# Kernel tuning notes

Hardware: AMD Instinct MI355X
Metric: run time of the kernel (lower is better)

Reference implementation:

```python
import jax, jax.numpy as jnp
import numpy as np

B, C_IN, C_OUT, H, W = 32, 256, 256, 56, 56
RATE = 0.5
K = int(C_OUT * (1.0 - RATE))  # 128 channels zeroed
BN_EPS = 1e-5


def setup_inputs() -> dict:
    key = jax.random.key(0)
    ks = jax.random.split(key, 4)
    return {
        "x": jax.random.normal(ks[0], (B, C_IN, H, W), dtype=jnp.float32),
        "conv_w": jax.random.normal(ks[1], (C_OUT, C_IN, 3, 3), dtype=jnp.float32) * 0.05,
        "gate_w": jax.random.normal(ks[2], (C_OUT, C_IN), dtype=jnp.float32) * 0.05,
        "gate_b": jnp.ones((C_OUT,), dtype=jnp.float32),
        "bn_gamma": jnp.ones((C_OUT,), dtype=jnp.float32),
        "bn_beta": jnp.zeros((C_OUT,), dtype=jnp.float32),
        "bn_mean": jnp.zeros((C_OUT,), dtype=jnp.float32),
        "bn_var": jnp.ones((C_OUT,), dtype=jnp.float32),
    }


def reference(x, conv_w, gate_w, gate_b, bn_gamma, bn_beta, bn_mean, bn_var):
    # conv2: 3x3, stride 1, padding 1, no bias  -> [B, C_OUT, H, W]
    y = jax.lax.conv_general_dilated(
        x, conv_w, window_strides=(1, 1), padding=((1, 1), (1, 1)),
        dimension_numbers=("NCHW", "OIHW", "NCHW"))
    # BatchNorm2d (eval mode: running stats)
    inv = bn_gamma / jnp.sqrt(bn_var + BN_EPS)
    y = y * inv[None, :, None, None] + (bn_beta - bn_mean * inv)[None, :, None, None]
    # use_relu=True
    y = jax.nn.relu(y)
    # gate: global abs-avg-pool -> linear -> relu   [B, C_OUT]
    s = jnp.mean(jnp.abs(x), axis=(2, 3))  # [B, C_IN]
    g = jax.nn.relu(s @ gate_w.T + gate_b)
    # zero the K smallest gate values per row (topk of -g), then renormalize
    _, idx = jax.lax.top_k(-g, K)  # indices of K smallest
    t = g.at[jnp.arange(B)[:, None], idx].set(0.0)
    t = t / jnp.sum(t, axis=1, keepdims=True) * C_OUT
    # broadcast channel mask
    return y * t[:, :, None, None]
```

## Files before the change

kernel.cpp:

```cpp
#include <hip/hip_runtime.h>
#include <hip/hip_bf16.h>
#include <cstdint>

typedef unsigned short ushort_t;
typedef unsigned int uint_t;
typedef __bf16 bf16x8 __attribute__((ext_vector_type(8)));
typedef float f32x4 __attribute__((ext_vector_type(4)));

#define B_SZ 32
#define C_IN 256
#define C_OUT 256
#define H_SZ 56
#define W_SZ 56
#define HW 3136
#define HP 58
#define WP 58
#define BN_EPS 1e-5f
#define K_ZERO 128

__device__ __forceinline__ ushort_t f2bf(float f) {
    unsigned int u = __builtin_bit_cast(unsigned int, f);
    unsigned int r = (u + 0x7fffu + ((u >> 16) & 1u)) >> 16;
    return (ushort_t)r;
}

__device__ __forceinline__ void load_lds16(const void* gptr, void* ldsptr) {
    __builtin_amdgcn_global_load_lds(
        (const __attribute__((address_space(1))) unsigned int*)(uintptr_t)gptr,
        (__attribute__((address_space(3))) unsigned int*)(uintptr_t)ldsptr,
        16, 0, 0);
}

__global__ __launch_bounds__(256) void prep_w_kernel(const float* __restrict__ w,
                                                     const float* __restrict__ gamma,
                                                     const float* __restrict__ beta,
                                                     const float* __restrict__ mean,
                                                     const float* __restrict__ var,
                                                     ushort_t* __restrict__ Wt,
                                                     float* __restrict__ bninv,
                                                     float* __restrict__ bnadd,
                                                     float* __restrict__ s) {
    int idx = blockIdx.x * 256 + threadIdx.x;
    if (idx < 9 * C_OUT * C_IN) {
        int tap = idx >> 16;
        int rem = idx & 65535;
        int co = rem >> 8, ci = rem & 255;
        Wt[idx] = f2bf(w[(size_t)(co * C_IN + ci) * 9 + tap]);
    }
    if (blockIdx.x < 32) s[idx] = 0.f;
    if (blockIdx.x == 32 && threadIdx.x < C_OUT) {
        int c = threadIdx.x;
        float inv = gamma[c] * rsqrtf(var[c] + BN_EPS);
        bninv[c] = inv;
        bnadd[c] = beta[c] - mean[c] * inv;
    }
}

__global__ __launch_bounds__(256) void prep_x_kernel(const float* __restrict__ x,
                                                     ushort_t* __restrict__ xbp,
                                                     float* __restrict__ s) {
    const int cit = blockIdx.x, h = blockIdx.y, b = blockIdx.z;
    __shared__ float tile[64][57];
    __shared__ float red2[256];
    const int t = threadIdx.x;
    const float* src = x + ((size_t)(b * C_IN + cit * 64) * H_SZ + h) * W_SZ;
    for (int i = t; i < 64 * 14; i += 256) {
        int ci = i / 14, w4 = (i - ci * 14) * 4;
        float4 v = *(const float4*)(src + (size_t)ci * HW + w4);
        tile[ci][w4] = v.x; tile[ci][w4 + 1] = v.y;
        tile[ci][w4 + 2] = v.z; tile[ci][w4 + 3] = v.w;
    }
    __syncthreads();
    {
        int ci = t & 63, wg = t >> 6;
        float a = 0.f;
#pragma unroll
        for (int j = 0; j < 14; j++) a += fabsf(tile[ci][wg * 14 + j]);
        red2[t] = a;
    }
    __syncthreads();
    if (t < 64) {
        float tot = red2[t] + red2[t + 64] + red2[t + 128] + red2[t + 192];
        atomicAdd(&s[b * C_IN + cit * 64 + t], tot * (1.0f / (float)HW));
    }
    const uint2 z2 = make_uint2(0u, 0u);
    for (int i = t; i < W_SZ * 16; i += 256) {
        int w = i >> 4, c4 = (i & 15) * 4;
        uint_t lo = (uint_t)f2bf(tile[c4][w])     | ((uint_t)f2bf(tile[c4 + 1][w]) << 16);
        uint_t hi = (uint_t)f2bf(tile[c4 + 2][w]) | ((uint_t)f2bf(tile[c4 + 3][w]) << 16);
        size_t dst = ((size_t)((b * HP + h + 1) * WP + (w + 1))) * C_IN + cit * 64 + c4;
        *(uint2*)&xbp[dst] = make_uint2(lo, hi);
    }
    if (t < 32) {
        int side = t >> 4, c4 = (t & 15) * 4;
        size_t dst = ((size_t)((b * HP + h + 1) * WP + side * 57)) * C_IN + cit * 64 + c4;
        *(uint2*)&xbp[dst] = z2;
    }
    if (h == 0 || h == 55) {
        int prow = (h == 0) ? 0 : 57;
        for (int i = t; i < 58 * 16; i += 256) {
            int w = i >> 4, c4 = (i & 15) * 4;
            size_t dst = ((size_t)((b * HP + prow) * WP + w)) * C_IN + cit * 64 + c4;
            *(uint2*)&xbp[dst] = z2;
        }
    }
}

__global__ __launch_bounds__(256) void gate_kernel(const float* __restrict__ s,
                                                   const float* __restrict__ gw,
                                                   const float* __restrict__ gb,
                                                   float* __restrict__ tscale) {
    const int b = blockIdx.x, t = threadIdx.x;
    __shared__ float sh_s[C_IN], sh_g[C_OUT], red[256];
    sh_s[t] = s[b * C_IN + t];
    __syncthreads();
    float acc = gb[t];
    const float* wr = gw + (size_t)t * C_IN;
    for (int ci = 0; ci < C_IN; ci++) acc += sh_s[ci] * wr[ci];
    float g = fmaxf(acc, 0.f);
    sh_g[t] = g;
    __syncthreads();
    int cnt = 0;
    for (int j = 0; j < C_OUT; j++) {
        float gj = sh_g[j];
        cnt += (gj < g) || (gj == g && j < t);
    }
    float tv = (cnt >= K_ZERO) ? g : 0.f;
    red[t] = tv;
    __syncthreads();
    for (int off = 128; off > 0; off >>= 1) {
        if (t < off) red[t] += red[t + off];
        __syncthreads();
    }
    tscale[b * C_OUT + t] = tv * ((float)C_OUT / red[0]);
}

__global__ __launch_bounds__(256, 3) void conv_kernel(const ushort_t* __restrict__ xbp,
                                                      const ushort_t* __restrict__ Wt,
                                                      const float* __restrict__ bninv,
                                                      const float* __restrict__ bnadd,
                                                      const float* __restrict__ tscale,
                                                      float* __restrict__ out) {
    __shared__ __align__(16) ushort_t As[128 * 64];
    __shared__ __align__(16) ushort_t Bs[128 * 64];
    const int t = threadIdx.x;
    const int bxr = blockIdx.x;
    const int bx = (bxr >> 4) * 8 + (bxr & 7);
    const int by = (bxr >> 3) & 1;
    const int lane = t & 63;
    const int wv = t >> 6;
    const int waveM = wv >> 1, waveN = wv & 1;

    const int srow = t >> 3;
    const int gxor8 = ((t & 7) ^ (srow & 7)) * 8;
    int arow[4], wrow[4];
#pragma unroll
    for (int i = 0; i < 4; i++) {
        int p = bx * 128 + i * 32 + srow;
        int b = p / HW;
        int r = p - b * HW;
        int hh = r / W_SZ, ww = r - hh * W_SZ;
        arow[i] = ((b * HP + hh + 1) * WP + (ww + 1)) * C_IN + gxor8;
        wrow[i] = (by * 128 + i * 32 + srow) * C_IN + gxor8;
    }
    ushort_t* ldsA = As + t * 8;
    ushort_t* ldsB = Bs + t * 8;

    int aoff[2][4], boff[2][4];
#pragma unroll
    for (int ks = 0; ks < 2; ks++) {
        int c = (lane >> 4) + ks * 4;
#pragma unroll
        for (int mt = 0; mt < 4; mt++) {
            int ra = waveM * 64 + mt * 16 + (lane & 15);
            aoff[ks][mt] = (ra * 8 + (c ^ (ra & 7))) * 16;
            int rb = waveN * 64 + mt * 16 + (lane & 15);
            boff[ks][mt] = (rb * 8 + (c ^ (rb & 7))) * 16;
        }
    }

    f32x4 acc[4][4];
#pragma unroll
    for (int i = 0; i < 4; i++)
#pragma unroll
        for (int j = 0; j < 4; j++) acc[i][j] = (f32x4){0.f, 0.f, 0.f, 0.f};

    const char* Ab = (const char*)As;
    const char* Bb = (const char*)Bs;

    for (int tap = 0; tap < 9; tap++) {
        const int doff = ((tap / 3 - 1) * WP + (tap % 3 - 1)) * C_IN;
        const int woff = tap * (C_OUT * C_IN);
#pragma unroll
        for (int cq = 0; cq < 4; cq++) {
            const int ci0 = cq * 64;
#pragma unroll
            for (int i = 0; i < 4; i++) {
                load_lds16(xbp + arow[i] + doff + ci0, ldsA + i * 2048);
                load_lds16(Wt + wrow[i] + woff + ci0, ldsB + i * 2048);
            }
            __syncthreads();
#pragma unroll
            for (int ks = 0; ks < 2; ks++) {
                bf16x8 af[4], bf[4];
#pragma unroll
                for (int mt = 0; mt < 4; mt++) af[mt] = *(const bf16x8*)(Ab + aoff[ks][mt]);
#pragma unroll
                for (int nt = 0; nt < 4; nt++) bf[nt] = *(const bf16x8*)(Bb + boff[ks][nt]);
#pragma unroll
                for (int mt = 0; mt < 4; mt++)
#pragma unroll
                    for (int nt = 0; nt < 4; nt++)
                        acc[mt][nt] = __builtin_amdgcn_mfma_f32_16x16x32_bf16(
                            af[mt], bf[nt], acc[mt][nt], 0, 0, 0);
            }
            __syncthreads();
        }
    }

#pragma unroll
    for (int mt = 0; mt < 4; mt++) {
        int p0 = bx * 128 + waveM * 64 + mt * 16 + (lane >> 4) * 4;
        int b = p0 / HW;
        int hw = p0 - b * HW;
#pragma unroll
        for (int nt = 0; nt < 4; nt++) {
            int co = by * 128 + waveN * 64 + nt * 16 + (lane & 15);
            float inv = bninv[co], add = bnadd[co], tsc = tscale[b * C_OUT + co];
            float4 o;
            o.x = fmaxf(acc[mt][nt][0] * inv + add, 0.f) * tsc;
            o.y = fmaxf(acc[mt][nt][1] * inv + add, 0.f) * tsc;
            o.z = fmaxf(acc[mt][nt][2] * inv + add, 0.f) * tsc;
            o.w = fmaxf(acc[mt][nt][3] * inv + add, 0.f) * tsc;
            *(float4*)(out + (size_t)(b * C_OUT + co) * HW + hw) = o;
        }
    }
}

extern "C" void kernel_launch(void* const* d_in, const int* in_sizes, int n_in,
                              void* d_out, int out_size, void* d_ws, size_t ws_size,
                              hipStream_t stream) {
    const float* x      = (const float*)d_in[0];
    const float* conv_w = (const float*)d_in[1];
    const float* gate_w = (const float*)d_in[2];
    const float* gate_b = (const float*)d_in[3];
    const float* bn_g   = (const float*)d_in[4];
    const float* bn_b   = (const float*)d_in[5];
    const float* bn_m   = (const float*)d_in[6];
    const float* bn_v   = (const float*)d_in[7];
    float* out = (float*)d_out;

    char* ws = (char*)d_ws;
    float*    s      = (float*)(ws + 0);
    float*    tscale = (float*)(ws + 32768);
    float*    bninv  = (float*)(ws + 65536);
    float*    bnadd  = (float*)(ws + 66560);
    ushort_t* Wt     = (ushort_t*)(ws + 67584);
    ushort_t* xbp    = (ushort_t*)(ws + 1247232);

    prep_w_kernel<<<2304, 256, 0, stream>>>(conv_w, bn_g, bn_b, bn_m, bn_v, Wt, bninv, bnadd, s);
    prep_x_kernel<<<dim3(4, 56, 32), 256, 0, stream>>>(x, xbp, s);
    gate_kernel<<<32, 256, 0, stream>>>(s, gate_w, gate_b, tscale);
    conv_kernel<<<1568, 256, 0, stream>>>(xbp, Wt, bninv, bnadd, tscale, out);
}
```

Baseline: 350.4 us.

## Reuse a padded input window in LDS across all nine conv taps

Each block now loads a 256-row window of padded input pixels for a 64-channel slice once, then runs all nine taps from shared memory by shifting the row offset. Before, the A tile was reloaded from global for every tap. Tiles no longer cross image boundaries: each image is split into 25 tiles, giving 1600 blocks, with a guard on the output store. The cost is a larger LDS footprint, which may cut occupancy, an extra barrier per tap for weight reloads, and some wasted rows in the last tile of each image.

Result: slower. 363.7 us (+3.8%).

```diff
diff --git a/kernel.cpp b/kernel.cpp
--- a/kernel.cpp
+++ b/kernel.cpp
@@ -15,6 +15,7 @@
 #define HW 3136
 #define HP 58
 #define WP 58
+#define HPWP 3364
 #define BN_EPS 1e-5f
 #define K_ZERO 128
 
@@ -141,41 +142,51 @@
                                                       const float* __restrict__ bnadd,
                                                       const float* __restrict__ tscale,
                                                       float* __restrict__ out) {
-    __shared__ __align__(16) ushort_t As[128 * 64];
+    __shared__ __align__(16) ushort_t Aw[256 * 64];
     __shared__ __align__(16) ushort_t Bs[128 * 64];
     const int t = threadIdx.x;
     const int bxr = blockIdx.x;
     const int bx = (bxr >> 4) * 8 + (bxr & 7);
     const int by = (bxr >> 3) & 1;
+    const int b = bx / 25;
+    const int ti = bx - b * 25;
     const int lane = t & 63;
     const int wv = t >> 6;
     const int waveM = wv >> 1, waveN = wv & 1;
 
+    const int r0 = ti * 128;
+    const int h0 = r0 / W_SZ, w0 = r0 - h0 * W_SZ;
+    const int padp0 = (h0 + 1) * WP + (w0 + 1);
+    const int g0l = min(padp0 - 59, HPWP - 256);
+
     const int srow = t >> 3;
     const int gxor8 = ((t & 7) ^ (srow & 7)) * 8;
-    int arow[4], wrow[4];
-#pragma unroll
-    for (int i = 0; i < 4; i++) {
-        int p = bx * 128 + i * 32 + srow;
-        int b = p / HW;
-        int r = p - b * HW;
+    const size_t abase = ((size_t)b * HPWP + g0l + srow) * C_IN + gxor8;
+    int wrowB[4];
+#pragma unroll
+    for (int i = 0; i < 4; i++)
+        wrowB[i] = (by * 128 + i * 32 + srow) * C_IN + gxor8;
+    ushort_t* ldsA = Aw + t * 8;
+    ushort_t* ldsB = Bs + t * 8;
+
+    int o_mt[4];
+#pragma unroll
+    for (int mt = 0; mt < 4; mt++) {
+        int r = r0 + waveM * 64 + mt * 16 + (lane & 15);
+        if (r >= HW) r = HW - 1;
         int hh = r / W_SZ, ww = r - hh * W_SZ;
-        arow[i] = ((b * HP + hh + 1) * WP + (ww + 1)) * C_IN + gxor8;
-        wrow[i] = (by * 128 + i * 32 + srow) * C_IN + gxor8;
-    }
-    ushort_t* ldsA = As + t * 8;
-    ushort_t* ldsB = Bs + t * 8;
-
-    int aoff[2][4], boff[2][4];
+        o_mt[mt] = (hh + 1) * WP + (ww + 1) - g0l;
+    }
+    const int q4 = (lane >> 4);
+
+    int boff[2][4];
 #pragma unroll
     for (int ks = 0; ks < 2; ks++) {
-        int c = (lane >> 4) + ks * 4;
-#pragma unroll
-        for (int mt = 0; mt < 4; mt++) {
-            int ra = waveM * 64 + mt * 16 + (lane & 15);
-            aoff[ks][mt] = (ra * 8 + (c ^ (ra & 7))) * 16;
-            int rb = waveN * 64 + mt * 16 + (lane & 15);
-            boff[ks][mt] = (rb * 8 + (c ^ (rb & 7))) * 16;
+        int c = q4 + ks * 4;
+#pragma unroll
+        for (int nt = 0; nt < 4; nt++) {
+            int rb = waveN * 64 + nt * 16 + (lane & 15);
+            boff[ks][nt] = (rb * 8 + (c ^ (rb & 7))) * 16;
         }
     }
 
@@ -185,28 +196,36 @@
 #pragma unroll
         for (int j = 0; j < 4; j++) acc[i][j] = (f32x4){0.f, 0.f, 0.f, 0.f};
 
-    const char* Ab = (const char*)As;
+    const char* Ab = (const char*)Aw;
     const char* Bb = (const char*)Bs;
 
-    for (int tap = 0; tap < 9; tap++) {
-        const int doff = ((tap / 3 - 1) * WP + (tap % 3 - 1)) * C_IN;
-        const int woff = tap * (C_OUT * C_IN);
-#pragma unroll
-        for (int cq = 0; cq < 4; cq++) {
-            const int ci0 = cq * 64;
-#pragma unroll
-            for (int i = 0; i < 4; i++) {
-                load_lds16(xbp + arow[i] + doff + ci0, ldsA + i * 2048);
-                load_lds16(Wt + wrow[i] + woff + ci0, ldsB + i * 2048);
-            }
-            __syncthreads();
+    for (int cq = 0; cq < 4; cq++) {
+        const int ci0 = cq * 64;
+#pragma unroll
+        for (int i = 0; i < 8; i++)
+            load_lds16(xbp + abase + (size_t)i * (32 * C_IN) + ci0, ldsA + i * 2048);
+#pragma unroll
+        for (int i = 0; i < 4; i++)
+            load_lds16(Wt + wrowB[i] + ci0, ldsB + i * 2048);
+        __syncthreads();
+
+        for (int tap = 0; tap < 9; tap++) {
+            const int dlt = (tap / 3 - 1) * WP + (tap % 3 - 1);
+            int aoff0[4];
+#pragma unroll
+            for (int mt = 0; mt < 4; mt++) {
+                int sp = o_mt[mt] + dlt;
+                aoff0[mt] = sp * 128 + ((q4 ^ (sp & 7)) << 4);
+            }
 #pragma unroll
             for (int ks = 0; ks < 2; ks++) {
                 bf16x8 af[4], bf[4];
 #pragma unroll
-                for (int mt = 0; mt < 4; mt++) af[mt] = *(const bf16x8*)(Ab + aoff[ks][mt]);
-#pragma unroll
-                for (int nt = 0; nt < 4; nt++) bf[nt] = *(const bf16x8*)(Bb + boff[ks][nt]);
+                for (int mt = 0; mt < 4; mt++)
+                    af[mt] = *(const bf16x8*)(Ab + (aoff0[mt] ^ (ks << 6)));
+#pragma unroll
+                for (int nt = 0; nt < 4; nt++)
+                    bf[nt] = *(const bf16x8*)(Bb + boff[ks][nt]);
 #pragma unroll
                 for (int mt = 0; mt < 4; mt++)
 #pragma unroll
@@ -215,24 +234,31 @@
                             af[mt], bf[nt], acc[mt][nt], 0, 0, 0);
             }
             __syncthreads();
+            if (tap < 8) {
+                const int woff = (tap + 1) * (C_OUT * C_IN) + ci0;
+#pragma unroll
+                for (int i = 0; i < 4; i++)
+                    load_lds16(Wt + wrowB[i] + woff, ldsB + i * 2048);
+                __syncthreads();
+            }
         }
     }
 
 #pragma unroll
     for (int mt = 0; mt < 4; mt++) {
-        int p0 = bx * 128 + waveM * 64 + mt * 16 + (lane >> 4) * 4;
-        int b = p0 / HW;
-        int hw = p0 - b * HW;
-#pragma unroll
-        for (int nt = 0; nt < 4; nt++) {
-            int co = by * 128 + waveN * 64 + nt * 16 + (lane & 15);
-            float inv = bninv[co], add = bnadd[co], tsc = tscale[b * C_OUT + co];
-            float4 o;
-            o.x = fmaxf(acc[mt][nt][0] * inv + add, 0.f) * tsc;
-            o.y = fmaxf(acc[mt][nt][1] * inv + add, 0.f) * tsc;
-            o.z = fmaxf(acc[mt][nt][2] * inv + add, 0.f) * tsc;
-            o.w = fmaxf(acc[mt][nt][3] * inv + add, 0.f) * tsc;
-            *(float4*)(out + (size_t)(b * C_OUT + co) * HW + hw) = o;
+        int r = r0 + waveM * 64 + mt * 16 + (lane >> 4) * 4;
+        if (r < HW) {
+#pragma unroll
+            for (int nt = 0; nt < 4; nt++) {
+                int co = by * 128 + waveN * 64 + nt * 16 + (lane & 15);
+                float inv = bninv[co], add = bnadd[co], tsc = tscale[b * C_OUT + co];
+                float4 o;
+                o.x = fmaxf(acc[mt][nt][0] * inv + add, 0.f) * tsc;
+                o.y = fmaxf(acc[mt][nt][1] * inv + add, 0.f) * tsc;
+                o.z = fmaxf(acc[mt][nt][2] * inv + add, 0.f) * tsc;
+                o.w = fmaxf(acc[mt][nt][3] * inv + add, 0.f) * tsc;
+                *(float4*)(out + (size_t)(b * C_OUT + co) * HW + r) = o;
+            }
         }
     }
 }
@@ -261,5 +287,5 @@
     prep_w_kernel<<<2304, 256, 0, stream>>>(conv_w, bn_g, bn_b, bn_m, bn_v, Wt, bninv, bnadd, s);
     prep_x_kernel<<<dim3(4, 56, 32), 256, 0, stream>>>(x, xbp, s);
     gate_kernel<<<32, 256, 0, stream>>>(s, gate_w, gate_b, tscale);
-    conv_kernel<<<1568, 256, 0, stream>>>(xbp, Wt, bninv, bnadd, tscale, out);
-}
+    conv_kernel<<<1600, 256, 0, stream>>>(xbp, Wt, bninv, bnadd, tscale, out);
+}
```

## Fuse weight prep into x prep and recompute gate inside conv blocks

Applied to the files above, without the earlier changes.

Merges the weight-conversion and BN-prep kernel into the input-prep kernel as an extra grid slice. Per-row partial abs-sums replace the atomics. The separate gate kernel is removed, and each conv block recomputes the gate (matvec, rank selection, normalisation) for its batch indices in a prologue. This cuts two launches and the serialization between them, at the cost of redundant gate work in every conv block before the GEMM starts.

New measurement: 386.3 us. 10.3% more time.

```diff
diff --git a/kernel.cpp b/kernel.cpp
--- a/kernel.cpp
+++ b/kernel.cpp
@@ -15,6 +15,7 @@
 #define HW 3136
 #define HP 58
 #define WP 58
+#define HPWP 3364
 #define BN_EPS 1e-5f
 #define K_ZERO 128
 
@@ -31,38 +32,37 @@
         16, 0, 0);
 }
 
-__global__ __launch_bounds__(256) void prep_w_kernel(const float* __restrict__ w,
-                                                     const float* __restrict__ gamma,
-                                                     const float* __restrict__ beta,
-                                                     const float* __restrict__ mean,
-                                                     const float* __restrict__ var,
-                                                     ushort_t* __restrict__ Wt,
-                                                     float* __restrict__ bninv,
-                                                     float* __restrict__ bnadd,
-                                                     float* __restrict__ s) {
-    int idx = blockIdx.x * 256 + threadIdx.x;
-    if (idx < 9 * C_OUT * C_IN) {
-        int tap = idx >> 16;
-        int rem = idx & 65535;
-        int co = rem >> 8, ci = rem & 255;
-        Wt[idx] = f2bf(w[(size_t)(co * C_IN + ci) * 9 + tap]);
-    }
-    if (blockIdx.x < 32) s[idx] = 0.f;
-    if (blockIdx.x == 32 && threadIdx.x < C_OUT) {
-        int c = threadIdx.x;
-        float inv = gamma[c] * rsqrtf(var[c] + BN_EPS);
-        bninv[c] = inv;
-        bnadd[c] = beta[c] - mean[c] * inv;
-    }
-}
-
-__global__ __launch_bounds__(256) void prep_x_kernel(const float* __restrict__ x,
-                                                     ushort_t* __restrict__ xbp,
-                                                     float* __restrict__ s) {
+__global__ __launch_bounds__(256) void prep_kernel(const float* __restrict__ x,
+                                                   const float* __restrict__ w,
+                                                   const float* __restrict__ gamma,
+                                                   const float* __restrict__ beta,
+                                                   const float* __restrict__ mean,
+                                                   const float* __restrict__ var,
+                                                   ushort_t* __restrict__ xbp,
+                                                   ushort_t* __restrict__ Wt,
+                                                   float* __restrict__ bninv,
+                                                   float* __restrict__ bnadd,
+                                                   float* __restrict__ s_part) {
+    const int t = threadIdx.x;
+    if (blockIdx.z == 32) {
+        const int cid = blockIdx.y * 4 + blockIdx.x;
+        for (int chunk = cid; chunk < 2304; chunk += 224) {
+            int idx = chunk * 256 + t;
+            int tap = idx >> 16;
+            int rem = idx & 65535;
+            int co = rem >> 8, ci = rem & 255;
+            Wt[idx] = f2bf(w[(size_t)(co * C_IN + ci) * 9 + tap]);
+        }
+        if (cid == 0) {
+            float inv = gamma[t] * rsqrtf(var[t] + BN_EPS);
+            bninv[t] = inv;
+            bnadd[t] = beta[t] - mean[t] * inv;
+        }
+        return;
+    }
     const int cit = blockIdx.x, h = blockIdx.y, b = blockIdx.z;
     __shared__ float tile[64][57];
     __shared__ float red2[256];
-    const int t = threadIdx.x;
     const float* src = x + ((size_t)(b * C_IN + cit * 64) * H_SZ + h) * W_SZ;
     for (int i = t; i < 64 * 14; i += 256) {
         int ci = i / 14, w4 = (i - ci * 14) * 4;
@@ -81,14 +81,14 @@
     __syncthreads();
     if (t < 64) {
         float tot = red2[t] + red2[t + 64] + red2[t + 128] + red2[t + 192];
-        atomicAdd(&s[b * C_IN + cit * 64 + t], tot * (1.0f / (float)HW));
+        s_part[((size_t)b * H_SZ + h) * C_IN + cit * 64 + t] = tot * (1.0f / (float)HW);
     }
     const uint2 z2 = make_uint2(0u, 0u);
     for (int i = t; i < W_SZ * 16; i += 256) {
-        int w = i >> 4, c4 = (i & 15) * 4;
-        uint_t lo = (uint_t)f2bf(tile[c4][w])     | ((uint_t)f2bf(tile[c4 + 1][w]) << 16);
-        uint_t hi = (uint_t)f2bf(tile[c4 + 2][w]) | ((uint_t)f2bf(tile[c4 + 3][w]) << 16);
-        size_t dst = ((size_t)((b * HP + h + 1) * WP + (w + 1))) * C_IN + cit * 64 + c4;
+        int w4 = i >> 4, c4 = (i & 15) * 4;
+        uint_t lo = (uint_t)f2bf(tile[c4][w4])     | ((uint_t)f2bf(tile[c4 + 1][w4]) << 16);
+        uint_t hi = (uint_t)f2bf(tile[c4 + 2][w4]) | ((uint_t)f2bf(tile[c4 + 3][w4]) << 16);
+        size_t dst = ((size_t)((b * HP + h + 1) * WP + (w4 + 1))) * C_IN + cit * 64 + c4;
         *(uint2*)&xbp[dst] = make_uint2(lo, hi);
     }
     if (t < 32) {
@@ -99,50 +99,24 @@
     if (h == 0 || h == 55) {
         int prow = (h == 0) ? 0 : 57;
         for (int i = t; i < 58 * 16; i += 256) {
-            int w = i >> 4, c4 = (i & 15) * 4;
-            size_t dst = ((size_t)((b * HP + prow) * WP + w)) * C_IN + cit * 64 + c4;
+            int w4 = i >> 4, c4 = (i & 15) * 4;
+            size_t dst = ((size_t)((b * HP + prow) * WP + w4)) * C_IN + cit * 64 + c4;
             *(uint2*)&xbp[dst] = z2;
         }
     }
-}
-
-__global__ __launch_bounds__(256) void gate_kernel(const float* __restrict__ s,
-                                                   const float* __restrict__ gw,
-                                                   const float* __restrict__ gb,
-                                                   float* __restrict__ tscale) {
-    const int b = blockIdx.x, t = threadIdx.x;
-    __shared__ float sh_s[C_IN], sh_g[C_OUT], red[256];
-    sh_s[t] = s[b * C_IN + t];
-    __syncthreads();
-    float acc = gb[t];
-    const float* wr = gw + (size_t)t * C_IN;
-    for (int ci = 0; ci < C_IN; ci++) acc += sh_s[ci] * wr[ci];
-    float g = fmaxf(acc, 0.f);
-    sh_g[t] = g;
-    __syncthreads();
-    int cnt = 0;
-    for (int j = 0; j < C_OUT; j++) {
-        float gj = sh_g[j];
-        cnt += (gj < g) || (gj == g && j < t);
-    }
-    float tv = (cnt >= K_ZERO) ? g : 0.f;
-    red[t] = tv;
-    __syncthreads();
-    for (int off = 128; off > 0; off >>= 1) {
-        if (t < off) red[t] += red[t + off];
-        __syncthreads();
-    }
-    tscale[b * C_OUT + t] = tv * ((float)C_OUT / red[0]);
 }
 
 __global__ __launch_bounds__(256, 3) void conv_kernel(const ushort_t* __restrict__ xbp,
                                                       const ushort_t* __restrict__ Wt,
                                                       const float* __restrict__ bninv,
                                                       const float* __restrict__ bnadd,
-                                                      const float* __restrict__ tscale,
+                                                      const float* __restrict__ s_part,
+                                                      const float* __restrict__ gw,
+                                                      const float* __restrict__ gb,
                                                       float* __restrict__ out) {
     __shared__ __align__(16) ushort_t As[128 * 64];
     __shared__ __align__(16) ushort_t Bs[128 * 64];
+    __shared__ float sh_gate[512];
     const int t = threadIdx.x;
     const int bxr = blockIdx.x;
     const int bx = (bxr >> 4) * 8 + (bxr & 7);
@@ -151,6 +125,42 @@
     const int wv = t >> 6;
     const int waveM = wv >> 1, waveN = wv & 1;
 
+    const int b0 = (bx * 128) / HW;
+    const int b1 = (bx * 128 + 127) / HW;
+    {
+        float* shs = (float*)As;
+        float* shg = (float*)As + 256;
+        float* red = (float*)As + 512;
+        const int nb = (b1 != b0) ? 2 : 1;
+        for (int pb = 0; pb < nb; pb++) {
+            const float* sp = s_part + ((size_t)(b0 + pb) * H_SZ) * C_IN + t;
+            float sv = 0.f;
+            for (int h = 0; h < H_SZ; h++) sv += sp[h * C_IN];
+            shs[t] = sv;
+            __syncthreads();
+            float acc = gb[t];
+            const float* wr = gw + (size_t)t * C_IN;
+            for (int ci = 0; ci < C_IN; ci++) acc += shs[ci] * wr[ci];
+            float g = fmaxf(acc, 0.f);
+            shg[t] = g;
+            __syncthreads();
+            int cnt = 0;
+            for (int j = 0; j < C_OUT; j++) {
+                float gj = shg[j];
+                cnt += (gj < g) || (gj == g && j < t);
+            }
+            float tv = (cnt >= K_ZERO) ? g : 0.f;
+            red[t] = tv;
+            __syncthreads();
+            for (int off = 128; off > 0; off >>= 1) {
+                if (t < off) red[t] += red[t + off];
+                __syncthreads();
+            }
+            sh_gate[pb * 256 + t] = tv * ((float)C_OUT / red[0]);
+            __syncthreads();
+        }
+    }
+
     const int srow = t >> 3;
     const int gxor8 = ((t & 7) ^ (srow & 7)) * 8;
     int arow[4], wrow[4];
@@ -223,10 +233,11 @@
         int p0 = bx * 128 + waveM * 64 + mt * 16 + (lane >> 4) * 4;
         int b = p0 / HW;
         int hw = p0 - b * HW;
+        const float* gsel = sh_gate + (b - b0) * 256;
 #pragma unroll
         for (int nt = 0; nt < 4; nt++) {
             int co = by * 128 + waveN * 64 + nt * 16 + (lane & 15);
-            float inv = bninv[co], add = bnadd[co], tsc = tscale[b * C_OUT + co];
+            float inv = bninv[co], add = bnadd[co], tsc = gsel[co];
             float4 o;
             o.x = fmaxf(acc[mt][nt][0] * inv + add, 0.f) * tsc;
             o.y = fmaxf(acc[mt][nt][1] * inv + add, 0.f) * tsc;
@@ -251,15 +262,14 @@
     float* out = (float*)d_out;
 
     char* ws = (char*)d_ws;
-    float*    s      = (float*)(ws + 0);
-    float*    tscale = (float*)(ws + 32768);
-    float*    bninv  = (float*)(ws + 65536);
-    float*    bnadd  = (float*)(ws + 66560);
-    ushort_t* Wt     = (ushort_t*)(ws + 67584);
-    ushort_t* xbp    = (ushort_t*)(ws + 1247232);
-
-    prep_w_kernel<<<2304, 256, 0, stream>>>(conv_w, bn_g, bn_b, bn_m, bn_v, Wt, bninv, bnadd, s);
-    prep_x_kernel<<<dim3(4, 56, 32), 256, 0, stream>>>(x, xbp, s);
-    gate_kernel<<<32, 256, 0, stream>>>(s, gate_w, gate_b, tscale);
-    conv_kernel<<<1568, 256, 0, stream>>>(xbp, Wt, bninv, bnadd, tscale, out);
-}
+    float*    bninv  = (float*)(ws + 0);
+    float*    bnadd  = (float*)(ws + 1024);
+    float*    s_part = (float*)(ws + 4096);
+    ushort_t* Wt     = (ushort_t*)(ws + 1839104);
+    ushort_t* xbp    = (ushort_t*)(ws + 3018752);
+
+    prep_kernel<<<dim3(4, 56, 33), 256, 0, stream>>>(x, conv_w, bn_g, bn_b, bn_m, bn_v,
+                                                     xbp, Wt, bninv, bnadd, s_part);
+    conv_kernel<<<1568, 256, 0, stream>>>(xbp, Wt, bninv, bnadd, s_part,
+                                          gate_w, gate_b, out);
+}
```
